# Optimization experiments

Measured on AMD Instinct MI355X. Metric: run time of the kernel, lower is better.

## Reference

```python
import jax, jax.numpy as jnp
import numpy as np

B, T, J = 128, 12, 17
HID, HEADS = 128, 8
LH, NC = 512, 500
E_IN = J * HID + 2 * HID  # 2432, matches hidden_channels*19 in the torch code

_pairs = [[15,13],[13,11],[16,14],[14,12],[11,12],[5,11],[6,12],[5,6],[5,7],
          [6,8],[7,9],[8,10],[1,2],[0,1],[0,2],[1,3],[2,4],[3,5],[4,6]]
_pairs = _pairs + [[b, a] for a, b in _pairs]
CONN = np.array(_pairs, dtype=np.int32).T  # [2, 38]: row0=source, row1=target


def setup_inputs():
    key = jax.random.key(0)
    ks = iter(jax.random.split(key, 48))
    def w(shape, s=0.05):
        return jax.random.normal(next(ks), shape, dtype=jnp.float32) * s
    inp = dict(
        pose1=jax.random.normal(next(ks), (B, T, J, 3), dtype=jnp.float32),
        pose2=jax.random.normal(next(ks), (B, T, J, 3), dtype=jnp.float32),
        W1=w((3, HEADS * HID)), a_src1=w((HEADS, HID)), a_dst1=w((HEADS, HID)),
        b1=jnp.zeros((HEADS * HID,), jnp.float32),
        W2=w((HEADS * HID, HEADS * HID)), a_src2=w((HEADS, HID)), a_dst2=w((HEADS, HID)),
        b2=jnp.zeros((HID,), jnp.float32),
        W_fc=w((2 * 19, HID)), b_fc=jnp.zeros((HID,), jnp.float32),
        bn_gamma=jnp.ones((T,), jnp.float32) + w((T,), 0.1),
        bn_beta=w((T,), 0.1), bn_mean=w((T,), 0.1), bn_var=jnp.ones((T,), jnp.float32),
        Wih_f=w((4 * LH, E_IN)), Whh_f=w((4 * LH, LH)),
        bih_f=jnp.zeros((4 * LH,), jnp.float32), bhh_f=jnp.zeros((4 * LH,), jnp.float32),
        Wih_b=w((4 * LH, E_IN)), Whh_b=w((4 * LH, LH)),
        bih_b=jnp.zeros((4 * LH,), jnp.float32), bhh_b=jnp.zeros((4 * LH,), jnp.float32),
        W_att=w((1, 2 * LH)), b_att=jnp.zeros((1,), jnp.float32),
        W_cls=w((NC, 2 * LH)), b_cls=jnp.zeros((NC,), jnp.float32),
        modal=0,
    )
    return inp


def reference(pose1, pose2, W1, a_src1, a_dst1, b1, W2, a_src2, a_dst2, b2,
              W_fc, b_fc, bn_gamma, bn_beta, bn_mean, bn_var,
              Wih_f, Whh_f, bih_f, bhh_f, Wih_b, Whh_b, bih_b, bhh_b,
              W_att, b_att, W_cls, b_cls, modal):
    c0 = jnp.asarray(CONN[0])
    c1 = jnp.asarray(CONN[1])

    def gat_conv(x, W, a_s, a_d, bias, esrc, edst, N, concat):
        # PyG GATConv (eval mode): self-loops already included in esrc/edst.
        H, C = a_s.shape
        h = (x @ W).reshape(N, H, C)
        al_s = jnp.einsum('nhc,hc->nh', h, a_s)   # [N,H]
        al_d = jnp.einsum('nhc,hc->nh', h, a_d)
        e = jax.nn.leaky_relu(al_s[esrc] + al_d[edst], 0.2)          # [E,H]
        m = jax.ops.segment_max(e, edst, num_segments=N)             # softmax per target
        ex = jnp.exp(e - m[edst])
        den = jax.ops.segment_sum(ex, edst, num_segments=N)
        a = ex / den[edst]
        out = jax.ops.segment_sum(a[:, :, None] * h[esrc], edst, num_segments=N)
        return (out.reshape(N, H * C) if concat else out.mean(axis=1)) + bias

    def gat_seq(pose):  # [B,T,J,3] -> [B,T,J*HID]
        Bq, Tq = pose.shape[0], pose.shape[1]
        N = Bq * J
        loops = jnp.arange(N, dtype=c0.dtype)
        esrc = jnp.concatenate([c0, loops])
        edst = jnp.concatenate([c1, loops])
        x = pose.transpose(1, 0, 2, 3).reshape(Tq, N, 3)
        def block(xf):
            hcat = jax.nn.elu(gat_conv(xf, W1, a_src1, a_dst1, b1, esrc, edst, N, True))
            return gat_conv(hcat, W2, a_src2, a_dst2, b2, esrc, edst, N, False)
        out = jax.vmap(block)(x)  # [T, N, HID]
        return out.reshape(Tq, Bq, J * HID).transpose(1, 0, 2)

    def edge_branch(pose):  # [B,T,J,3] -> [B,T,2*HID]
        Bq, Tq = pose.shape[0], pose.shape[1]
        p = pose.reshape(-1, J, 3)
        v = p[:, c1, :2] - p[:, c0, :2]                              # [BT,38,2]
        ef = jnp.stack([jnp.linalg.norm(v, axis=-1),
                        jnp.arctan2(v[..., 1], v[..., 0])], axis=-1)  # [BT,38,2]
        ef = ef.reshape(-1, 2 * 19) @ W_fc + b_fc                    # view(-1,38): [2*BT,128]
        return ef.reshape(Bq, Tq, 2 * HID)

    if modal == 0:
        f1 = jnp.concatenate([gat_seq(pose1), edge_branch(pose1)], axis=-1)
        f2 = jnp.concatenate([gat_seq(pose2), edge_branch(pose2)], axis=-1)
        feats = jnp.concatenate([f1, f2], axis=0)
    else:
        feats = jnp.concatenate([gat_seq(pose1), edge_branch(pose1)], axis=-1)

    # BatchNorm1d(12), eval mode, channels = time dim 1
    inv = jax.lax.rsqrt(bn_var + 1e-5)
    feats = (feats - bn_mean[None, :, None]) * (inv * bn_gamma)[None, :, None] + bn_beta[None, :, None]

    def lstm_dir(x, Wih, Whh, bih, bhh, reverse):
        pre = jnp.einsum('btd,gd->btg', x, Wih) + bih + bhh
        Bq = x.shape[0]
        init = (jnp.zeros((Bq, LH), x.dtype), jnp.zeros((Bq, LH), x.dtype))
        def step(carry, xt):
            h, c = carry
            g = xt + h @ Whh.T
            i, f, gg, o = jnp.split(g, 4, axis=-1)  # torch gate order i,f,g,o
            c = jax.nn.sigmoid(f) * c + jax.nn.sigmoid(i) * jnp.tanh(gg)
            h = jax.nn.sigmoid(o) * jnp.tanh(c)
            return (h, c), h
        _, ys = jax.lax.scan(step, init, pre.transpose(1, 0, 2), reverse=reverse)
        return ys.transpose(1, 0, 2)

    lout = jnp.concatenate([
        lstm_dir(feats, Wih_f, Whh_f, bih_f, bhh_f, False),
        lstm_dir(feats, Wih_b, Whh_b, bih_b, bhh_b, True)], axis=-1)  # [2B,T,1024]

    attw = jax.nn.softmax(lout @ W_att.T + b_att, axis=1)
    attended = jnp.sum(lout * attw, axis=1)   # [2B,1024]
    logits = attended @ W_cls.T + b_cls       # [2B,NC]
    return (attended, logits)
```

## Files before the change

### kernel.cpp

```cpp
#include <hip/hip_runtime.h>
#include <hip/hip_bf16.h>
#include <math.h>

#define B_    128
#define T_    12
#define J_    17
#define HID_  128
#define LH_   512
#define NC_   500

typedef short  bf16x8 __attribute__((ext_vector_type(8)));
typedef ushort u16x8  __attribute__((ext_vector_type(8)));
typedef float  f32x4  __attribute__((ext_vector_type(4)));

__constant__ int d_c0[38] = {15,13,16,14,11,5,6,5,5,6,7,8,1,0,0,1,2,3,4,
                             13,11,14,12,12,11,12,6,7,8,9,10,2,1,2,3,4,5,6};
__constant__ int d_c1[38] = {13,11,14,12,12,11,12,6,7,8,9,10,2,1,2,3,4,5,6,
                             15,13,16,14,11,5,6,5,5,6,7,8,1,0,0,1,2,3,4};

__device__ __forceinline__ float lrelu02(float x){ return x > 0.f ? x : 0.2f*x; }
__device__ __forceinline__ float sigmoidf_(float x){ return 1.f/(1.f+__expf(-x)); }
__device__ __forceinline__ ushort f2bf(float f){
  uint32_t u = __builtin_bit_cast(uint32_t, f);
  uint32_t r = (u + 0x7fffu + ((u >> 16) & 1u)) >> 16;
  return (ushort)r;
}
__device__ __forceinline__ void llds16(const ushort* g, ushort* l){
  __builtin_amdgcn_global_load_lds(
      (const __attribute__((address_space(1))) void*)g,
      (__attribute__((address_space(3))) void*)l,
      16, 0, 0);
}

__global__ __launch_bounds__(256) void k_front1(const float* __restrict__ W2,
    const float* __restrict__ Wih_f, const float* __restrict__ Wih_b,
    const float* __restrict__ Whh_f, const float* __restrict__ Whh_b,
    const float* __restrict__ pose1, const float* __restrict__ pose2,
    const float* __restrict__ W1,
    const float* __restrict__ a_s1, const float* __restrict__ a_d1,
    const float* __restrict__ W_fc, const float* __restrict__ b_fc,
    const float* __restrict__ bn_g, const float* __restrict__ bn_b,
    const float* __restrict__ bn_m, const float* __restrict__ bn_v,
    ushort* __restrict__ W2mT, ushort* __restrict__ W2tb,
    ushort* __restrict__ Wbf, ushort* __restrict__ Whh_pbf,
    float* __restrict__ rawh_p, float* __restrict__ al_s_p, float* __restrict__ al_d_p,
    ushort* __restrict__ fb)
{
  __shared__ ushort sh[64][68];
  __shared__ float rh[1024];
  __shared__ float nrm[38], ang[38];
  int tid = threadIdx.x;
  int bx = blockIdx.x;
  if (bx < 512){
    int idx = bx*256 + tid;
    int c = idx >> 10, k = idx & 1023;
    float s = 0.f;
    #pragma unroll
    for (int h = 0; h < 8; h++) s += W2[k*1024 + h*128 + c];
    W2mT[idx] = f2bf(s * 0.125f);
  } else if (bx < 768){
    int b2x = bx - 512;
    int k0 = (b2x >> 4)*64, n0 = (b2x & 15)*64;
    #pragma unroll
    for (int q = 0; q < 16; q++){
      int idx = tid + q*256;
      int kk = idx >> 6, nn = idx & 63;
      sh[nn][kk] = f2bf(W2[(size_t)(k0+kk)*1024 + n0+nn]);
    }
    __syncthreads();
    #pragma unroll
    for (int q = 0; q < 16; q++){
      int idx = tid + q*256;
      int nn = idx >> 6, kk = idx & 63;
      W2tb[(size_t)(n0+nn)*1024 + k0+kk] = sh[nn][kk];
    }
  } else if (bx < 10496){
    const int S = 2048*2432;
    int i4 = (bx - 768)*256 + tid;
    int idx = i4*4;
    if (idx >= 2*S) return;
    const float* src = (idx < S) ? (Wih_f + idx) : (Wih_b + (idx - S));
    float4 v = *(const float4*)src;
    ushort4 o;
    o.x = f2bf(v.x); o.y = f2bf(v.y); o.z = f2bf(v.z); o.w = f2bf(v.w);
    *(ushort4*)(Wbf + idx) = o;
  } else if (bx < 11520){
    int i = (bx - 10496)*256 + tid;
    int base = i*8;
    int dir = base >> 20;
    int rem = base & 1048575;
    int n_p = rem >> 9, k8 = rem & 511;
    int u = n_p >> 2, g = n_p & 3;
    const float* src = (dir ? Whh_b : Whh_f) + ((size_t)(g*512+u))*512 + k8;
    float4 v0 = *(const float4*)src;
    float4 v1 = *(const float4*)(src+4);
    ushort av[8] = {f2bf(v0.x),f2bf(v0.y),f2bf(v0.z),f2bf(v0.w),
                    f2bf(v1.x),f2bf(v1.y),f2bf(v1.z),f2bf(v1.w)};
    *(u16x8*)(Whh_pbf + (size_t)base) = *(u16x8*)av;
  } else if (bx < 11928){
    int id = bx - 11520;
    int p = id / 204, tn = id % 204;
    const float* pose = p ? pose2 : pose1;
    float* rawh = rawh_p + p*208896;
    const float* xp = pose + tn*3;
    float x0 = xp[0], x1 = xp[1], x2 = xp[2];
    #pragma unroll
    for (int j = 0; j < 4; j++){
      int c = tid + j*256;
      float v = x0*W1[c] + x1*W1[1024+c] + x2*W1[2048+c];
      rh[c] = v;
      rawh[tn*1024 + c] = v;
    }
    __syncthreads();
    int o = tid >> 4, l = tid & 15;
    int h = o & 7;
    const float* av = ((o < 8) ? a_s1 : a_d1) + h*128;
    const float* hv = rh + h*128;
    float s = 0.f;
    #pragma unroll
    for (int q = 0; q < 8; q++) s += hv[l + q*16] * av[l + q*16];
    #pragma unroll
    for (int off = 1; off < 16; off <<= 1) s += __shfl_xor(s, off, 64);
    if (l == 0) ((o < 8) ? al_s_p : al_d_p)[p*2048 + tn*8 + h] = s;
  } else {
    int id = bx - 11928;
    int p = id / 1536, bt = id % 1536;
    const float* pose = p ? pose2 : pose1;
    int b = bt/12, t = bt%12;
    if (tid < 38){
      const float* pb = pose + ((b*12 + t)*17)*3;
      int s = d_c0[tid], d = d_c1[tid];
      float vx = pb[d*3+0] - pb[s*3+0];
      float vy = pb[d*3+1] - pb[s*3+1];
      nrm[tid] = sqrtf(vx*vx + vy*vy);
      ang[tid] = atan2f(vy, vx);
    }
    __syncthreads();
    float inv = rsqrtf(bn_v[t] + 1e-5f);
    float sc = inv*bn_g[t], shv = bn_b[t] - bn_m[t]*sc;
    int c = tid & 127, blk = tid >> 7;
    float acc = b_fc[c];
    #pragma unroll
    for (int j = 0; j < 19; j++){
      int e = blk*19 + j;
      acc += nrm[e]*W_fc[(2*j)*128 + c] + ang[e]*W_fc[(2*j+1)*128 + c];
    }
    fb[(((size_t)(p*128+b))*12 + t)*2432 + 2176 + blk*128 + c] = f2bf(acc*sc + shv);
  }
}

#define GLDK 40
__global__ __launch_bounds__(256) void k_front2(
    const float* __restrict__ pose1, const float* __restrict__ pose2,
    const float* __restrict__ W1, const float* __restrict__ b1,
    const ushort* __restrict__ W2mT, const float* __restrict__ b2,
    const float* __restrict__ bn_g, const float* __restrict__ bn_b,
    const float* __restrict__ bn_m, const float* __restrict__ bn_v,
    const float* __restrict__ rawh_p,
    const float* __restrict__ al_s_p, const float* __restrict__ al_d_p,
    ushort* __restrict__ hcat_bf, ushort* __restrict__ fb)
{
  __shared__ ushort As[64*GLDK];
  __shared__ ushort Bs[128*GLDK];
  __shared__ float sx[64][3];
  int tid = threadIdx.x;
  int bx = blockIdx.x;
  if (bx < 408){
    int p = bx / 204, r = bx % 204;
    const float* rawh = rawh_p + p*208896;
    const float* al_s = al_s_p + p*2048;
    const float* al_d = al_d_p + p*2048;
    int t = r/17, dst = r%17;
    int base = t*17;
    int row = p*204 + base + dst;
    #pragma unroll
    for (int j = 0; j < 4; j++){
      int c = tid + j*256, h = c >> 7;
      float ad = al_d[(base+dst)*8 + h];
      float eself = lrelu02(al_s[(base+dst)*8 + h] + ad);
      float m = eself;
      for (int e = 0; e < 38; e++) if (d_c1[e] == dst)
        m = fmaxf(m, lrelu02(al_s[(base+d_c0[e])*8 + h] + ad));
      float w = __expf(eself - m);
      float den = w;
      float acc = w * rawh[(base+dst)*1024 + c];
      for (int e = 0; e < 38; e++) if (d_c1[e] == dst){
        float v = __expf(lrelu02(al_s[(base+d_c0[e])*8 + h] + ad) - m);
        den += v;
        acc += v * rawh[(base+d_c0[e])*1024 + c];
      }
      float o = acc/den + b1[c];
      hcat_bf[(size_t)row*1024 + c] = f2bf(o > 0.f ? o : __expf(o) - 1.f);
    }
    return;
  }
  int id = bx - 408;
  int n0 = (id % 34) * 64;
  int t  = (id / 34) % 12;
  int p  = id / 408;
  const float* pose = p ? pose2 : pose1;
  if (tid < 192){
    int nd = tid/3, k = tid%3;
    int n = n0+nd, b = n/17, jj = n%17;
    sx[nd][k] = pose[((b*12 + t)*17 + jj)*3 + k];
  }
  __syncthreads();
  float inv = rsqrtf(bn_v[t] + 1e-5f);
  float sc = inv*bn_g[t], shv = bn_b[t] - bn_m[t]*sc;
  int wave = tid >> 6, lane = tid & 63;
  int wm = (wave >> 1)*32, wn = (wave & 1)*64;
  int fr = lane & 15, fg = lane >> 4;
  int and_ = tid >> 2, ak8 = (tid & 3)*8;
  int brow = tid >> 1, bk16 = (tid & 1)*16;
  float ax0 = sx[and_][0], ax1 = sx[and_][1], ax2 = sx[and_][2];

  f32x4 acc[2][4];
  #pragma unroll
  for (int m = 0; m < 2; m++)
    #pragma unroll
    for (int n = 0; n < 4; n++) acc[m][n] = (f32x4){0.f,0.f,0.f,0.f};

  u16x8 vb0 = *(const u16x8*)(W2mT + brow*1024 + bk16);
  u16x8 vb1 = *(const u16x8*)(W2mT + brow*1024 + bk16 + 8);

  for (int k0 = 0; k0 < 1024; k0 += 32){
    ushort av[8];
    #pragma unroll
    for (int q = 0; q < 8; q++){
      int k = k0 + ak8 + q;
      float hv = ax0*W1[k] + ax1*W1[1024+k] + ax2*W1[2048+k] + b1[k];
      hv = hv > 0.f ? hv : __expf(hv) - 1.f;
      av[q] = f2bf(hv);
    }
    if (k0) __syncthreads();
    *(u16x8*)(&As[and_*GLDK + ak8]) = *(u16x8*)av;
    *(u16x8*)(&Bs[brow*GLDK + bk16])     = vb0;
    *(u16x8*)(&Bs[brow*GLDK + bk16 + 8]) = vb1;
    __syncthreads();
    if (k0 + 32 < 1024){
      vb0 = *(const u16x8*)(W2mT + brow*1024 + k0 + 32 + bk16);
      vb1 = *(const u16x8*)(W2mT + brow*1024 + k0 + 32 + bk16 + 8);
    }
    bf16x8 af[2], bfv[4];
    #pragma unroll
    for (int m = 0; m < 2; m++)
      af[m] = *(const bf16x8*)(&As[(wm + m*16 + fr)*GLDK + fg*8]);
    #pragma unroll
    for (int n = 0; n < 4; n++)
      bfv[n] = *(const bf16x8*)(&Bs[(wn + n*16 + fr)*GLDK + fg*8]);
    #pragma unroll
    for (int m = 0; m < 2; m++)
      #pragma unroll
      for (int n = 0; n < 4; n++)
        acc[m][n] = __builtin_amdgcn_mfma_f32_16x16x32_bf16(af[m], bfv[n], acc[m][n], 0, 0, 0);
  }

  #pragma unroll
  for (int m = 0; m < 2; m++){
    #pragma unroll
    for (int n = 0; n < 4; n++){
      int col = wn + n*16 + fr;
      float bb = b2[col];
      #pragma unroll
      for (int j = 0; j < 4; j++){
        int node = n0 + wm + m*16 + fg*4 + j;
        int b = node/17, jj = node%17;
        float val = (acc[m][n][j] + bb)*sc + shv;
        fb[(((size_t)(p*128+b))*12 + t)*2432 + jj*128 + col] = f2bf(val);
      }
    }
  }
}

#define PLDK 40
__global__ __launch_bounds__(256) void k_gat2sp(
    const ushort* __restrict__ hcat_bf,
    const ushort* __restrict__ W2tb,
    const float* __restrict__ a_s, const float* __restrict__ a_d,
    float* __restrict__ h2s,
    float* __restrict__ al_s_p, float* __restrict__ al_d_p)
{
  __shared__ ushort As[64*PLDK];
  __shared__ ushort Bs[128*PLDK];
  __shared__ float alred[64][2][2];
  int tid = threadIdx.x;
  int bm = blockIdx.y * 64;
  int bn = blockIdx.x * 128;
  int hh = blockIdx.x;
  int wave = tid >> 6, lane = tid & 63;
  int wm = (wave >> 1)*32, wn = (wave & 1)*64;
  int fr = lane & 15, fg = lane >> 4;
  int arow = tid >> 2, ak8 = (tid & 3)*8;
  int brow = tid >> 1, bk16 = (tid & 1)*16;

  f32x4 acc[2][4];
  #pragma unroll
  for (int m = 0; m < 2; m++)
    #pragma unroll
    for (int n = 0; n < 4; n++) acc[m][n] = (f32x4){0.f,0.f,0.f,0.f};

  const ushort* ga = hcat_bf + (size_t)(bm+arow)*1024 + ak8;
  const ushort* gb = W2tb + (size_t)(bn+brow)*1024 + bk16;
  u16x8 va  = *(const u16x8*)ga;
  u16x8 vb0 = *(const u16x8*)gb;
  u16x8 vb1 = *(const u16x8*)(gb + 8);

  for (int k0 = 0; k0 < 1024; k0 += 32){
    if (k0) __syncthreads();
    *(u16x8*)(&As[arow*PLDK + ak8]) = va;
    *(u16x8*)(&Bs[brow*PLDK + bk16])     = vb0;
    *(u16x8*)(&Bs[brow*PLDK + bk16 + 8]) = vb1;
    __syncthreads();
    if (k0 + 32 < 1024){
      va  = *(const u16x8*)(ga + k0 + 32);
      vb0 = *(const u16x8*)(gb + k0 + 32);
      vb1 = *(const u16x8*)(gb + k0 + 40);
    }
    bf16x8 af[2], bfv[4];
    #pragma unroll
    for (int m = 0; m < 2; m++)
      af[m] = *(const bf16x8*)(&As[(wm + m*16 + fr)*PLDK + fg*8]);
    #pragma unroll
    for (int n = 0; n < 4; n++)
      bfv[n] = *(const bf16x8*)(&Bs[(wn + n*16 + fr)*PLDK + fg*8]);
    #pragma unroll
    for (int m = 0; m < 2; m++)
      #pragma unroll
      for (int n = 0; n < 4; n++)
        acc[m][n] = __builtin_amdgcn_mfma_f32_16x16x32_bf16(af[m], bfv[n], acc[m][n], 0, 0, 0);
  }

  #pragma unroll
  for (int m = 0; m < 2; m++){
    #pragma unroll
    for (int n = 0; n < 4; n++){
      int col = bn + wn + n*16 + fr;
      #pragma unroll
      for (int j = 0; j < 4; j++){
        int row = bm + wm + m*16 + fg*4 + j;
        if (row < 408) h2s[(size_t)row*1024 + col] = acc[m][n][j];
      }
    }
  }

  float avs[4], avd[4];
  #pragma unroll
  for (int n = 0; n < 4; n++){
    avs[n] = a_s[hh*128 + wn + n*16 + fr];
    avd[n] = a_d[hh*128 + wn + n*16 + fr];
  }
  #pragma unroll
  for (int m = 0; m < 2; m++){
    #pragma unroll
    for (int j = 0; j < 4; j++){
      float ps = 0.f, pd = 0.f;
      #pragma unroll
      for (int n = 0; n < 4; n++){
        ps += acc[m][n][j]*avs[n];
        pd += acc[m][n][j]*avd[n];
      }
      #pragma unroll
      for (int off = 1; off < 16; off <<= 1){
        ps += __shfl_xor(ps, off, 64);
        pd += __shfl_xor(pd, off, 64);
      }
      if (fr == 0){
        int rl = wm + m*16 + fg*4 + j;
        alred[rl][wave & 1][0] = ps;
        alred[rl][wave & 1][1] = pd;
      }
    }
  }
  __syncthreads();
  if (tid < 128){
    int rl = tid & 63, kind = tid >> 6;
    int grow = bm + rl;
    if (grow < 408){
      float v = alred[rl][0][kind] + alred[rl][1][kind];
      int p = grow / 204, tn = grow % 204;
      (kind ? al_d_p : al_s_p)[p*2048 + tn*8 + hh] = v;
    }
  }
}

__global__ void k_gat2_agg(const float* __restrict__ h2s_p, const float* __restrict__ al_s_p,
    const float* __restrict__ al_d_p, const float* __restrict__ b2,
    const float* __restrict__ bn_g, const float* __restrict__ bn_b,
    const float* __restrict__ bn_m, const float* __restrict__ bn_v,
    ushort* __restrict__ fb){
  int p = blockIdx.x / 204, r = blockIdx.x % 204;
  const float* h2s = h2s_p + p*208896;
  const float* al_s = al_s_p + p*2048;
  const float* al_d = al_d_p + p*2048;
  int t = r/17, dst = r%17;
  int base = t*17, c = threadIdx.x;
  float sum = 0.f;
  for (int h = 0; h < 8; h++){
    float ad = al_d[(base+dst)*8 + h];
    float eself = lrelu02(al_s[(base+dst)*8 + h] + ad);
    float m = eself;
    for (int e = 0; e < 38; e++) if (d_c1[e] == dst)
      m = fmaxf(m, lrelu02(al_s[(base+d_c0[e])*8 + h] + ad));
    float w = __expf(eself - m), den = w;
    float acc = w * h2s[(base+dst)*1024 + h*128 + c];
    for (int e = 0; e < 38; e++) if (d_c1[e] == dst){
      float v = __expf(lrelu02(al_s[(base+d_c0[e])*8 + h] + ad) - m);
      den += v;
      acc += v * h2s[(base+d_c0[e])*1024 + h*128 + c];
    }
    sum += acc/den;
  }
  float inv = rsqrtf(bn_v[t] + 1e-5f);
  float sc = inv*bn_g[t], shv = bn_b[t] - bn_m[t]*sc;
  float val = (sum*0.125f + b2[c])*sc + shv;
  fb[(((size_t)(p*128))*12 + t)*2432 + dst*128 + c] = f2bf(val);
}

__global__ __launch_bounds__(256) void k_proj_mfma(
    const ushort* __restrict__ Abf,
    const ushort* __restrict__ Wbf,
    const float* __restrict__ bih_f, const float* __restrict__ bhh_f,
    const float* __restrict__ bih_b, const float* __restrict__ bhh_b,
    float* __restrict__ pre)
{
  __shared__ ushort As[128*32];
  __shared__ ushort Bs[128*32];
  int tid = threadIdx.x;
  int bm = blockIdx.y * 128;
  int dir = blockIdx.x >> 4;
  int bn = (blockIdx.x & 15) * 128;
  const ushort* W = Wbf + (size_t)dir * (2048*2432);
  const float* bi = dir ? bih_b : bih_f;
  const float* bh = dir ? bhh_b : bhh_f;
  float* C = pre + (size_t)dir * 6291456;

  int wave = tid >> 6, lane = tid & 63;
  int wm = (wave >> 1) * 64, wn = (wave & 1) * 64;
  int fr = lane & 15, fg = lane >> 4;

  int grow = tid >> 2, gks = (tid & 3) * 8;
  const ushort* gaBase = Abf + (size_t)(bm + grow)*2432 + gks;
  const ushort* gbBase = W   + (size_t)(bn + grow)*2432 + gks;
  ushort* ldsA0 = &As[(wave*16)*32];
  ushort* ldsA1 = &As[(64 + wave*16)*32];
  ushort* ldsB0 = &Bs[(wave*16)*32];
  ushort* ldsB1 = &Bs[(64 + wave*16)*32];

  f32x4 acc[4][4];
  #pragma unroll
  for (int i = 0; i < 4; i++)
    #pragma unroll
    for (int j = 0; j < 4; j++) acc[i][j] = (f32x4){0.f,0.f,0.f,0.f};

  for (int k0 = 0; k0 < 2432; k0 += 32){
    __syncthreads();
    llds16(gaBase + k0,             ldsA0);
    llds16(gaBase + k0 + 64*2432,   ldsA1);
    llds16(gbBase + k0,             ldsB0);
    llds16(gbBase + k0 + 64*2432,   ldsB1);
    __syncthreads();
    bf16x8 af[4], bfv[4];
    #pragma unroll
    for (int m = 0; m < 4; m++)
      af[m] = *(const bf16x8*)(&As[(wm + m*16 + fr)*32 + fg*8]);
    #pragma unroll
    for (int n = 0; n < 4; n++)
      bfv[n] = *(const bf16x8*)(&Bs[(wn + n*16 + fr)*32 + fg*8]);
    #pragma unroll
    for (int m = 0; m < 4; m++)
      #pragma unroll
      for (int n = 0; n < 4; n++)
        acc[m][n] = __builtin_amdgcn_mfma_f32_16x16x32_bf16(af[m], bfv[n], acc[m][n], 0, 0, 0);
  }

  #pragma unroll
  for (int m = 0; m < 4; m++){
    #pragma unroll
    for (int n = 0; n < 4; n++){
      int col = bn + wn + n*16 + fr;
      float bsum = bi[col] + bh[col];
      #pragma unroll
      for (int j = 0; j < 4; j++){
        int row = bm + wm + m*16 + fg*4 + j;
        C[(size_t)row*2048 + col] = acc[m][n][j] + bsum;
      }
    }
  }
}

__global__ __launch_bounds__(512) void k_lstm_step(
    ushort* __restrict__ hbf, const ushort* __restrict__ Whh_pbf,
    const float* __restrict__ pre, float* __restrict__ cbuf,
    float* __restrict__ lout, int s)
{
  int dir = blockIdx.z;
  int bm = blockIdx.y * 64;
  int bn = blockIdx.x * 64;
  int tCur = dir ? (11 - s) : s;
  int tid = threadIdx.x, wave = tid >> 6, lane = tid & 63;
  int kg = wave >> 2, wv = wave & 3;
  int fr = lane & 15, fg = lane >> 4;
  __shared__ ushort As[2][64*32];
  __shared__ ushort Bs[2][64*32];
  __shared__ float sg[64][68];
  f32x4 acc[4];
  #pragma unroll
  for (int n = 0; n < 4; n++) acc[n] = (f32x4){0.f,0.f,0.f,0.f};

  if (s > 0){
    const ushort* hA = hbf + ((size_t)((s&1)*2 + dir))*131072;
    const ushort* WB = Whh_pbf + (size_t)dir*1048576;
    int rsub = lane >> 2, kl = (lane & 3)*8;
    const ushort* gA = hA + (size_t)(bm + wv*16 + rsub)*512 + kg*256 + kl;
    const ushort* gB = WB + (size_t)(bn + wv*16 + rsub)*512 + kg*256 + kl;
    ushort* lA = &As[kg][(wv*16)*32];
    ushort* lB = &Bs[kg][(wv*16)*32];
    for (int k0 = 0; k0 < 256; k0 += 32){
      if (k0) __syncthreads();
      llds16(gA + k0, lA);
      llds16(gB + k0, lB);
      __syncthreads();
      bf16x8 af = *(const bf16x8*)(&As[kg][(wv*16 + fr)*32 + fg*8]);
      #pragma unroll
      for (int n = 0; n < 4; n++){
        bf16x8 bfv = *(const bf16x8*)(&Bs[kg][(n*16 + fr)*32 + fg*8]);
        acc[n] = __builtin_amdgcn_mfma_f32_16x16x32_bf16(af, bfv, acc[n], 0, 0, 0);
      }
    }
    __syncthreads();
  }
  if (kg == 0){
    #pragma unroll
    for (int n = 0; n < 4; n++)
      #pragma unroll
      for (int j = 0; j < 4; j++)
        sg[wv*16 + fg*4 + j][n*16 + fr] = acc[n][j];
  }
  __syncthreads();
  if (kg == 1){
    #pragma unroll
    for (int n = 0; n < 4; n++)
      #pragma unroll
      for (int j = 0; j < 4; j++)
        sg[wv*16 + fg*4 + j][n*16 + fr] += acc[n][j];
  }
  __syncthreads();

  int ul = tid & 15, rb = tid >> 4;
  int u = (bn >> 2) + ul;
  ushort* hw = hbf + ((size_t)(((s&1)^1)*2 + dir))*131072;
  #pragma unroll
  for (int q = 0; q < 2; q++){
    int r = rb + q*32, b = bm + r;
    const float* pb = pre + (size_t)dir*6291456 + ((size_t)b*12 + tCur)*2048;
    float gi = sg[r][ul*4+0] + pb[u];
    float gf = sg[r][ul*4+1] + pb[512+u];
    float gg = sg[r][ul*4+2] + pb[1024+u];
    float go = sg[r][ul*4+3] + pb[1536+u];
    float cP = (s > 0) ? cbuf[dir*131072 + b*512 + u] : 0.f;
    float cN = sigmoidf_(gf)*cP + sigmoidf_(gi)*tanhf(gg);
    float h = sigmoidf_(go)*tanhf(cN);
    cbuf[dir*131072 + b*512 + u] = cN;
    lout[((size_t)b*12 + tCur)*1024 + dir*512 + u] = h;
    hw[(size_t)b*512 + u] = f2bf(h);
  }
}

__global__ __launch_bounds__(256) void k_gemm_bt(
    const float* __restrict__ A, int lda,
    const float* __restrict__ B, int ldb,
    float* __restrict__ C, int ldc,
    int M, int N, int K,
    const float* __restrict__ bias1)
{
  __shared__ float As[16][68];
  __shared__ float Bs[16][68];
  int tid = threadIdx.x;
  int bm = blockIdx.y*64, bn = blockIdx.x*64;
  int lr = tid >> 2, lk = (tid & 3) << 2;
  int tx = tid & 15, ty = tid >> 4;
  float acc[4][4] = {{0.f}};
  for (int k0 = 0; k0 < K; k0 += 16){
    float4 va = make_float4(0.f,0.f,0.f,0.f), vb = make_float4(0.f,0.f,0.f,0.f);
    int ar = bm + lr;
    if (ar < M) va = *(const float4*)(A + (size_t)ar*lda + k0 + lk);
    int br = bn + lr;
    if (br < N) vb = *(const float4*)(B + (size_t)br*ldb + k0 + lk);
    As[lk+0][lr]=va.x; As[lk+1][lr]=va.y; As[lk+2][lr]=va.z; As[lk+3][lr]=va.w;
    Bs[lk+0][lr]=vb.x; Bs[lk+1][lr]=vb.y; Bs[lk+2][lr]=vb.z; Bs[lk+3][lr]=vb.w;
    __syncthreads();
    #pragma unroll
    for (int kk = 0; kk < 16; kk++){
      float4 av = *(const float4*)(&As[kk][ty*4]);
      float4 bv = *(const float4*)(&Bs[kk][tx*4]);
      acc[0][0] += av.x*bv.x; acc[0][1] += av.x*bv.y; acc[0][2] += av.x*bv.z; acc[0][3] += av.x*bv.w;
      acc[1][0] += av.y*bv.x; acc[1][1] += av.y*bv.y; acc[1][2] += av.y*bv.z; acc[1][3] += av.y*bv.w;
      acc[2][0] += av.z*bv.x; acc[2][1] += av.z*bv.y; acc[2][2] += av.z*bv.z; acc[2][3] += av.z*bv.w;
      acc[3][0] += av.w*bv.x; acc[3][1] += av.w*bv.y; acc[3][2] += av.w*bv.z; acc[3][3] += av.w*bv.w;
    }
    __syncthreads();
  }
  #pragma unroll
  for (int i = 0; i < 4; i++){
    int r = bm + ty*4 + i;
    if (r >= M) continue;
    #pragma unroll
    for (int j = 0; j < 4; j++){
      int cc = bn + tx*4 + j;
      if (cc >= N) continue;
      float v = acc[i][j];
      if (bias1) v += bias1[cc];
      C[(size_t)r*ldc + cc] = v;
    }
  }
}

__global__ __launch_bounds__(256) void k_attention(const float* __restrict__ lout,
    const float* __restrict__ W_att, float* __restrict__ attended){
  int b = blockIdx.x, tid = threadIdx.x;
  __shared__ float part[256*12];
  __shared__ float sc[12];
  float p[12];
  #pragma unroll
  for (int t = 0; t < 12; t++) p[t] = 0.f;
  #pragma unroll
  for (int j = 0; j < 4; j++){
    int c = tid + j*256;
    float w = W_att[c];
    #pragma unroll
    for (int t = 0; t < 12; t++) p[t] += lout[((size_t)b*12 + t)*1024 + c] * w;
  }
  #pragma unroll
  for (int t = 0; t < 12; t++) part[tid*12 + t] = p[t];
  __syncthreads();
  if (tid < 12){
    float s = 0.f;
    for (int i = 0; i < 256; i++) s += part[i*12 + tid];
    sc[tid] = s;
  }
  __syncthreads();
  float m = sc[0];
  #pragma unroll
  for (int t = 1; t < 12; t++) m = fmaxf(m, sc[t]);
  float wt[12], den = 0.f;
  #pragma unroll
  for (int t = 0; t < 12; t++){ wt[t] = __expf(sc[t] - m); den += wt[t]; }
  float inv = 1.f/den;
  #pragma unroll
  for (int j = 0; j < 4; j++){
    int c = tid + j*256;
    float a = 0.f;
    #pragma unroll
    for (int t = 0; t < 12; t++) a += wt[t]*lout[((size_t)b*12 + t)*1024 + c];
    attended[(size_t)b*1024 + c] = a*inv;
  }
}

extern "C" void kernel_launch(void* const* d_in, const int* in_sizes, int n_in,
                              void* d_out, int out_size, void* d_ws, size_t ws_size,
                              hipStream_t stream)
{
  const float* pose1 = (const float*)d_in[0];
  const float* pose2 = (const float*)d_in[1];
  const float* W1    = (const float*)d_in[2];
  const float* a_src1= (const float*)d_in[3];
  const float* a_dst1= (const float*)d_in[4];
  const float* b1    = (const float*)d_in[5];
  const float* W2    = (const float*)d_in[6];
  const float* a_src2= (const float*)d_in[7];
  const float* a_dst2= (const float*)d_in[8];
  const float* b2    = (const float*)d_in[9];
  const float* W_fc  = (const float*)d_in[10];
  const float* b_fc  = (const float*)d_in[11];
  const float* bn_g  = (const float*)d_in[12];
  const float* bn_b  = (const float*)d_in[13];
  const float* bn_m  = (const float*)d_in[14];
  const float* bn_v  = (const float*)d_in[15];
  const float* Wih_f = (const float*)d_in[16];
  const float* Whh_f = (const float*)d_in[17];
  const float* bih_f = (const float*)d_in[18];
  const float* bhh_f = (const float*)d_in[19];
  const float* Wih_b = (const float*)d_in[20];
  const float* Whh_b = (const float*)d_in[21];
  const float* bih_b = (const float*)d_in[22];
  const float* bhh_b = (const float*)d_in[23];
  const float* W_att = (const float*)d_in[24];
  const float* W_cls = (const float*)d_in[26];
  const float* b_cls = (const float*)d_in[27];
  (void)in_sizes; (void)n_in; (void)out_size; (void)ws_size;

  float* ws = (float*)d_ws;
  ushort* Wbf     = (ushort*)ws;
  ushort* Whh_pbf = (ushort*)(ws + 4980736);
  ushort* W2tb    = (ushort*)(ws + 6029312);
  ushort* W2mT    = (ushort*)(ws + 6553600);
  float* pre      = ws + 7471104;
  float* rawh_p   = pre;
  float* R        = ws + 20054016;
  ushort* fb      = (ushort*)R;
  float* h2s      = R + 3735552;
  ushort* hcat_bf = (ushort*)(R + 4153344);
  float* alB      = R + 4382720;
  float* al1s = alB, *al1d = alB + 4096, *al2s = alB + 8192, *al2d = alB + 12288;
  ushort* hbf = (ushort*)R;
  float* cbuf = R + 262144;
  float* lout = R + 524288;

  float* attended = (float*)d_out;
  float* logits   = attended + 262144;

  k_front1<<<15000, 256, 0, stream>>>(W2, Wih_f, Wih_b, Whh_f, Whh_b,
      pose1, pose2, W1, a_src1, a_dst1, W_fc, b_fc,
      bn_g, bn_b, bn_m, bn_v,
      W2mT, W2tb, Wbf, Whh_pbf, rawh_p, al1s, al1d, fb);

  k_front2<<<1224, 256, 0, stream>>>(pose1, pose2, W1, b1, W2mT, b2,
      bn_g, bn_b, bn_m, bn_v, rawh_p, al1s, al1d, hcat_bf, fb);

  k_gat2sp<<<dim3(8,7), 256, 0, stream>>>(hcat_bf, W2tb, a_src2, a_dst2,
                                          h2s, al2s, al2d);
  k_gat2_agg<<<408, 128, 0, stream>>>(h2s, al2s, al2d, b2,
                                      bn_g, bn_b, bn_m, bn_v, fb);

  k_proj_mfma<<<dim3(32, 24), 256, 0, stream>>>(fb, Wbf,
      bih_f, bhh_f, bih_b, bhh_b, pre);

  for (int s = 0; s < 12; s++)
    k_lstm_step<<<dim3(32,4,2), 512, 0, stream>>>(hbf, Whh_pbf, pre, cbuf, lout, s);

  k_attention<<<256, 256, 0, stream>>>(lout, W_att, attended);
  k_gemm_bt<<<dim3(8,4), 256, 0, stream>>>(attended, 1024, W_cls, 1024, logits, 500,
                                           256, 500, 1024, b_cls);
}
```

Before: 370.5 us.

## Pre-pack Whh into MFMA fragment layout and store LSTM input projections in bf16

The recurrent weight matrix is rearranged at conversion time into the exact per-lane MFMA B-fragment order. Each LSTM step wave can then load its weight fragments straight from global memory into registers, with no LDS staging buffer. The input-projection output is also stored as bf16 instead of fp32, which halves its write traffic and the per-step gate reads. The trade-offs are some loss of precision in the pre-activation gates and reliance on the cache for weight fragments that each wave reloads.

```diff
diff --git a/kernel.cpp b/kernel.cpp
--- a/kernel.cpp
+++ b/kernel.cpp
@@ -24,6 +24,10 @@
   uint32_t u = __builtin_bit_cast(uint32_t, f);
   uint32_t r = (u + 0x7fffu + ((u >> 16) & 1u)) >> 16;
   return (ushort)r;
+}
+__device__ __forceinline__ float bf2f(ushort u){
+  uint32_t v = ((uint32_t)u) << 16;
+  return __builtin_bit_cast(float, v);
 }
 __device__ __forceinline__ void llds16(const ushort* g, ushort* l){
   __builtin_amdgcn_global_load_lds(
@@ -42,7 +46,7 @@
     const float* __restrict__ bn_g, const float* __restrict__ bn_b,
     const float* __restrict__ bn_m, const float* __restrict__ bn_v,
     ushort* __restrict__ W2mT, ushort* __restrict__ W2tb,
-    ushort* __restrict__ Wbf, ushort* __restrict__ Whh_pbf,
+    ushort* __restrict__ Wbf, ushort* __restrict__ Whh_pk,
     float* __restrict__ rawh_p, float* __restrict__ al_s_p, float* __restrict__ al_d_p,
     ushort* __restrict__ fb)
 {
@@ -88,15 +92,24 @@
     int i = (bx - 10496)*256 + tid;
     int base = i*8;
     int dir = base >> 20;
-    int rem = base & 1048575;
-    int n_p = rem >> 9, k8 = rem & 511;
-    int u = n_p >> 2, g = n_p & 3;
-    const float* src = (dir ? Whh_b : Whh_f) + ((size_t)(g*512+u))*512 + k8;
+    int idx8 = (base & 1048575) >> 3;
+    int lane = idx8 & 63;
+    int t1 = idx8 >> 6;
+    int n  = t1 & 3;
+    int t2 = t1 >> 2;
+    int kk = t2 & 7;
+    int t3 = t2 >> 3;
+    int kg = t3 & 1;
+    int nb = t3 >> 1;
+    int col = nb*64 + n*16 + (lane & 15);
+    int u = col >> 2, g = col & 3;
+    int k = kg*256 + kk*32 + (lane >> 4)*8;
+    const float* src = (dir ? Whh_b : Whh_f) + ((size_t)(g*512+u))*512 + k;
     float4 v0 = *(const float4*)src;
     float4 v1 = *(const float4*)(src+4);
     ushort av[8] = {f2bf(v0.x),f2bf(v0.y),f2bf(v0.z),f2bf(v0.w),
                     f2bf(v1.x),f2bf(v1.y),f2bf(v1.z),f2bf(v1.w)};
-    *(u16x8*)(Whh_pbf + (size_t)base) = *(u16x8*)av;
+    *(u16x8*)(Whh_pk + (size_t)base) = *(u16x8*)av;
   } else if (bx < 11928){
     int id = bx - 11520;
     int p = id / 204, tn = id % 204;
@@ -421,7 +434,7 @@
     const ushort* __restrict__ Wbf,
     const float* __restrict__ bih_f, const float* __restrict__ bhh_f,
     const float* __restrict__ bih_b, const float* __restrict__ bhh_b,
-    float* __restrict__ pre)
+    ushort* __restrict__ pre_bf)
 {
   __shared__ ushort As[128*32];
   __shared__ ushort Bs[128*32];
@@ -432,7 +445,7 @@
   const ushort* W = Wbf + (size_t)dir * (2048*2432);
   const float* bi = dir ? bih_b : bih_f;
   const float* bh = dir ? bhh_b : bhh_f;
-  float* C = pre + (size_t)dir * 6291456;
+  ushort* C = pre_bf + (size_t)dir * 6291456;
 
   int wave = tid >> 6, lane = tid & 63;
   int wm = (wave >> 1) * 64, wn = (wave & 1) * 64;
@@ -482,15 +495,15 @@
       #pragma unroll
       for (int j = 0; j < 4; j++){
         int row = bm + wm + m*16 + fg*4 + j;
-        C[(size_t)row*2048 + col] = acc[m][n][j] + bsum;
+        C[(size_t)row*2048 + col] = f2bf(acc[m][n][j] + bsum);
       }
     }
   }
 }
 
 __global__ __launch_bounds__(512) void k_lstm_step(
-    ushort* __restrict__ hbf, const ushort* __restrict__ Whh_pbf,
-    const float* __restrict__ pre, float* __restrict__ cbuf,
+    ushort* __restrict__ hbf, const ushort* __restrict__ Whh_pk,
+    const ushort* __restrict__ pre_bf, float* __restrict__ cbuf,
     float* __restrict__ lout, int s)
 {
   int dir = blockIdx.z;
@@ -501,7 +514,6 @@
   int kg = wave >> 2, wv = wave & 3;
   int fr = lane & 15, fg = lane >> 4;
   __shared__ ushort As[2][64*32];
-  __shared__ ushort Bs[2][64*32];
   __shared__ float sg[64][68];
   f32x4 acc[4];
   #pragma unroll
@@ -509,23 +521,25 @@
 
   if (s > 0){
     const ushort* hA = hbf + ((size_t)((s&1)*2 + dir))*131072;
-    const ushort* WB = Whh_pbf + (size_t)dir*1048576;
     int rsub = lane >> 2, kl = (lane & 3)*8;
     const ushort* gA = hA + (size_t)(bm + wv*16 + rsub)*512 + kg*256 + kl;
-    const ushort* gB = WB + (size_t)(bn + wv*16 + rsub)*512 + kg*256 + kl;
     ushort* lA = &As[kg][(wv*16)*32];
-    ushort* lB = &Bs[kg][(wv*16)*32];
-    for (int k0 = 0; k0 < 256; k0 += 32){
-      if (k0) __syncthreads();
-      llds16(gA + k0, lA);
-      llds16(gB + k0, lB);
+    const ushort* wb = Whh_pk + (size_t)dir*1048576
+                     + (size_t)blockIdx.x*32768 + kg*16384 + lane*8;
+    #pragma unroll
+    for (int kk = 0; kk < 8; kk++){
+      if (kk) __syncthreads();
+      bf16x8 bfv0 = *(const bf16x8*)(wb + kk*2048 + 0*512);
+      bf16x8 bfv1 = *(const bf16x8*)(wb + kk*2048 + 1*512);
+      bf16x8 bfv2 = *(const bf16x8*)(wb + kk*2048 + 2*512);
+      bf16x8 bfv3 = *(const bf16x8*)(wb + kk*2048 + 3*512);
+      llds16(gA + kk*32, lA);
       __syncthreads();
       bf16x8 af = *(const bf16x8*)(&As[kg][(wv*16 + fr)*32 + fg*8]);
-      #pragma unroll
-      for (int n = 0; n < 4; n++){
-        bf16x8 bfv = *(const bf16x8*)(&Bs[kg][(n*16 + fr)*32 + fg*8]);
-        acc[n] = __builtin_amdgcn_mfma_f32_16x16x32_bf16(af, bfv, acc[n], 0, 0, 0);
-      }
+      acc[0] = __builtin_amdgcn_mfma_f32_16x16x32_bf16(af, bfv0, acc[0], 0, 0, 0);
+      acc[1] = __builtin_amdgcn_mfma_f32_16x16x32_bf16(af, bfv1, acc[1], 0, 0, 0);
+      acc[2] = __builtin_amdgcn_mfma_f32_16x16x32_bf16(af, bfv2, acc[2], 0, 0, 0);
+      acc[3] = __builtin_amdgcn_mfma_f32_16x16x32_bf16(af, bfv3, acc[3], 0, 0, 0);
     }
     __syncthreads();
   }
@@ -552,11 +566,11 @@
   #pragma unroll
   for (int q = 0; q < 2; q++){
     int r = rb + q*32, b = bm + r;
-    const float* pb = pre + (size_t)dir*6291456 + ((size_t)b*12 + tCur)*2048;
-    float gi = sg[r][ul*4+0] + pb[u];
-    float gf = sg[r][ul*4+1] + pb[512+u];
-    float gg = sg[r][ul*4+2] + pb[1024+u];
-    float go = sg[r][ul*4+3] + pb[1536+u];
+    const ushort* pb = pre_bf + (size_t)dir*6291456 + ((size_t)b*12 + tCur)*2048;
+    float gi = sg[r][ul*4+0] + bf2f(pb[u]);
+    float gf = sg[r][ul*4+1] + bf2f(pb[512+u]);
+    float gg = sg[r][ul*4+2] + bf2f(pb[1024+u]);
+    float go = sg[r][ul*4+3] + bf2f(pb[1536+u]);
     float cP = (s > 0) ? cbuf[dir*131072 + b*512 + u] : 0.f;
     float cN = sigmoidf_(gf)*cP + sigmoidf_(gi)*tanhf(gg);
     float h = sigmoidf_(go)*tanhf(cN);
@@ -691,11 +705,11 @@
 
   float* ws = (float*)d_ws;
   ushort* Wbf     = (ushort*)ws;
-  ushort* Whh_pbf = (ushort*)(ws + 4980736);
+  ushort* Whh_pk  = (ushort*)(ws + 4980736);
   ushort* W2tb    = (ushort*)(ws + 6029312);
   ushort* W2mT    = (ushort*)(ws + 6553600);
-  float* pre      = ws + 7471104;
-  float* rawh_p   = pre;
+  ushort* pre_bf  = (ushort*)(ws + 7471104);
+  float* rawh_p   = ws + 7471104;
   float* R        = ws + 20054016;
   ushort* fb      = (ushort*)R;
   float* h2s      = R + 3735552;
@@ -712,7 +726,7 @@
   k_front1<<<15000, 256, 0, stream>>>(W2, Wih_f, Wih_b, Whh_f, Whh_b,
       pose1, pose2, W1, a_src1, a_dst1, W_fc, b_fc,
       bn_g, bn_b, bn_m, bn_v,
-      W2mT, W2tb, Wbf, Whh_pbf, rawh_p, al1s, al1d, fb);
+      W2mT, W2tb, Wbf, Whh_pk, rawh_p, al1s, al1d, fb);
 
   k_front2<<<1224, 256, 0, stream>>>(pose1, pose2, W1, b1, W2mT, b2,
       bn_g, bn_b, bn_m, bn_v, rawh_p, al1s, al1d, hcat_bf, fb);
@@ -723,10 +737,10 @@
                                       bn_g, bn_b, bn_m, bn_v, fb);
 
   k_proj_mfma<<<dim3(32, 24), 256, 0, stream>>>(fb, Wbf,
-      bih_f, bhh_f, bih_b, bhh_b, pre);
+      bih_f, bhh_f, bih_b, bhh_b, pre_bf);
 
   for (int s = 0; s < 12; s++)
-    k_lstm_step<<<dim3(32,4,2), 512, 0, stream>>>(hbf, Whh_pbf, pre, cbuf, lout, s);
+    k_lstm_step<<<dim3(32,4,2), 512, 0, stream>>>(hbf, Whh_pk, pre_bf, cbuf, lout, s);
 
   k_attention<<<256, 256, 0, stream>>>(lout, W_att, attended);
   k_gemm_bt<<<dim3(8,4), 256, 0, stream>>>(attended, 1024, W_cls, 1024, logits, 500,
```

After: 371.9 us. Within noise of the previous version (+0.4%).
